# Kernel tuning notes

Measured on AMD Instinct MI355X. Metric: run time of the kernel, lower is better.

The kernel has to match this reference:

```python
import jax, jax.numpy as jnp
import numpy as np

N_NODES = 100000
N_EDGES = 1250000
IN_DIM = 64
HID_DIM = 64
EDGE_DIM = 10
BN_EPS = 1e-5


def setup_inputs() -> dict:
    key = jax.random.key(0)
    ks = jax.random.split(key, 10)
    x = jax.random.normal(ks[0], (N_NODES, IN_DIM), dtype=jnp.float32)
    edge_index = jax.random.randint(ks[1], (2, N_EDGES), 0, N_NODES, dtype=jnp.int64)
    edge_attr = jax.random.normal(ks[2], (N_EDGES, EDGE_DIM), dtype=jnp.float32)
    # GINEConv edge projection Linear(edge_dim=10 -> indim)
    W_edge = jax.random.normal(ks[3], (EDGE_DIM, IN_DIM), dtype=jnp.float32) * (1.0 / np.sqrt(EDGE_DIM))
    b_edge = jnp.zeros((IN_DIM,), dtype=jnp.float32)
    # MLP: Linear(indim, hiddendim) -> ReLU -> Linear(hiddendim, hiddendim)
    W1 = jax.random.normal(ks[4], (IN_DIM, HID_DIM), dtype=jnp.float32) * (1.0 / np.sqrt(IN_DIM))
    b1 = jnp.zeros((HID_DIM,), dtype=jnp.float32)
    W2 = jax.random.normal(ks[5], (HID_DIM, HID_DIM), dtype=jnp.float32) * (1.0 / np.sqrt(HID_DIM))
    b2 = jnp.zeros((HID_DIM,), dtype=jnp.float32)
    # BatchNorm1d affine params
    bn_gamma = jnp.ones((HID_DIM,), dtype=jnp.float32)
    bn_beta = jnp.zeros((HID_DIM,), dtype=jnp.float32)
    return {"x": x, "edge_index": edge_index, "edge_attr": edge_attr,
            "W_edge": W_edge, "b_edge": b_edge, "W1": W1, "b1": b1,
            "W2": W2, "b2": b2, "bn_gamma": bn_gamma, "bn_beta": bn_beta}


def reference(x, edge_index, edge_attr, W_edge, b_edge, W1, b1, W2, b2, bn_gamma, bn_beta):
    src, dst = edge_index[0], edge_index[1]
    # message: ReLU(x_j + lin(edge_attr))  [E, indim]
    msg = jax.nn.relu(x[src] + edge_attr @ W_edge + b_edge)
    # sum-aggregate into destination nodes  [N, indim]
    aggr = jax.ops.segment_sum(msg, dst, num_segments=N_NODES)
    # GIN update: nn((1+eps)*x + aggr), eps=0
    h = x + aggr
    h = jax.nn.relu(h @ W1 + b1) @ W2 + b2
    # outer ReLU then BatchNorm1d (training-mode batch stats)
    h = jax.nn.relu(h)
    mean = jnp.mean(h, axis=0)
    var = jnp.var(h, axis=0)
    out = (h - mean) * jax.lax.rsqrt(var + BN_EPS) * bn_gamma + bn_beta
    return out
```

## Files before the change

kernel.cpp:

```cpp
#include <hip/hip_runtime.h>

#define N_NODES 100000
#define N_EDGES 1250000
#define DIM 64
#define EDGE_DIM 10
#define BN_EPS 1e-5f

#define SCAN_CHUNK 1024
#define NB_SCAN ((N_NODES + SCAN_CHUNK - 1) / SCAN_CHUNK)

#define DEG_OFF    0
#define SUMS_OFF_I (DEG_OFF + N_NODES)
#define OFFS_OFF   (SUMS_OFF_I + 256)
#define CUR_OFF    (OFFS_OFF + N_NODES)
#define BSUM_OFF   (CUR_OFF + N_NODES)
#define WH_OFF     (BSUM_OFF + 128)
#define REC_OFF    (WH_OFF + 4096)

typedef __attribute__((ext_vector_type(8))) short short8v;
typedef __attribute__((ext_vector_type(4))) float f32x4v;

__device__ __forceinline__ unsigned f2bf(float f) {
    unsigned b = __float_as_uint(f);
    return (b + 0x7FFFu + ((b >> 16) & 1u)) >> 16;
}

__device__ __forceinline__ short8v pack8(float4 a, float4 b) {
    short8v r;
    r[0] = (short)f2bf(a.x); r[1] = (short)f2bf(a.y);
    r[2] = (short)f2bf(a.z); r[3] = (short)f2bf(a.w);
    r[4] = (short)f2bf(b.x); r[5] = (short)f2bf(b.y);
    r[6] = (short)f2bf(b.z); r[7] = (short)f2bf(b.w);
    return r;
}

extern "C" __global__ __launch_bounds__(256)
void prep_kernel(const float* __restrict__ x, unsigned short* __restrict__ xh,
                 const int* __restrict__ ei, int* __restrict__ deg)
{
    int t = blockIdx.x * 256 + threadIdx.x;
    int stride = gridDim.x * 256;
    for (int i = t; i < N_NODES * DIM / 4; i += stride) {
        float4 v = ((const float4*)x)[i];
        uint2 p;
        p.x = f2bf(v.x) | (f2bf(v.y) << 16);
        p.y = f2bf(v.z) | (f2bf(v.w) << 16);
        ((uint2*)xh)[i] = p;
    }
    for (int e = t; e < N_EDGES; e += stride) {
        unsigned d = (unsigned)ei[N_EDGES + e];
        d = d < N_NODES ? d : (N_NODES - 1);
        atomicAdd(&deg[d], 1);
    }
}

extern "C" __global__ __launch_bounds__(256)
void scan_bsum_kernel(const int* __restrict__ deg, int* __restrict__ bsum,
                      const float* __restrict__ W1, const float* __restrict__ W2,
                      unsigned* __restrict__ wh)
{
    __shared__ int sw[4];
    int tid = threadIdx.x;
    if (blockIdx.x == 0) {
        for (int g = tid; g < 4096; g += 256) {
            int layer = g >> 11;
            int r  = g & 2047;
            int kb = r >> 10;
            int r2 = r & 1023;
            int cg = r2 >> 8;
            int r3 = r2 & 255;
            int ln = r3 >> 2;
            int ip = r3 & 3;
            int k0 = kb * 32 + (ln >> 4) * 8 + 2 * ip;
            int c  = cg * 16 + (ln & 15);
            const float* W = layer ? W2 : W1;
            unsigned lo = f2bf(W[k0 * DIM + c]);
            unsigned hi = f2bf(W[(k0 + 1) * DIM + c]);
            wh[g] = lo | (hi << 16);
        }
    }
    int base = blockIdx.x * SCAN_CHUNK + tid * 4;
    int s = 0;
    #pragma unroll
    for (int j = 0; j < 4; ++j) {
        int idx = base + j;
        if (idx < N_NODES) s += deg[idx];
    }
    #pragma unroll
    for (int m = 1; m < 64; m <<= 1) s += __shfl_xor(s, m, 64);
    if ((tid & 63) == 0) sw[tid >> 6] = s;
    __syncthreads();
    if (tid == 0) bsum[blockIdx.x] = sw[0] + sw[1] + sw[2] + sw[3];
}

extern "C" __global__ __launch_bounds__(128)
void scan_top_kernel(int* __restrict__ bsum)
{
    __shared__ int s[128];
    int tid = threadIdx.x;
    int v = (tid < NB_SCAN) ? bsum[tid] : 0;
    s[tid] = v;
    __syncthreads();
    #pragma unroll
    for (int off = 1; off < 128; off <<= 1) {
        int t = (tid >= off) ? s[tid - off] : 0;
        __syncthreads();
        s[tid] += t;
        __syncthreads();
    }
    if (tid < NB_SCAN) bsum[tid] = s[tid] - v;
}

extern "C" __global__ __launch_bounds__(256)
void scan_final_kernel(const int* __restrict__ deg, const int* __restrict__ bsum,
                       int* __restrict__ offs, int* __restrict__ cur)
{
    __shared__ int s[256];
    int tid = threadIdx.x;
    int base = blockIdx.x * SCAN_CHUNK + tid * 4;
    int d[4];
    #pragma unroll
    for (int j = 0; j < 4; ++j) {
        int idx = base + j;
        d[j] = (idx < N_NODES) ? deg[idx] : 0;
    }
    int tot = d[0] + d[1] + d[2] + d[3];
    s[tid] = tot;
    __syncthreads();
    #pragma unroll
    for (int off = 1; off < 256; off <<= 1) {
        int t = (tid >= off) ? s[tid - off] : 0;
        __syncthreads();
        s[tid] += t;
        __syncthreads();
    }
    int b = bsum[blockIdx.x] + s[tid] - tot;
    #pragma unroll
    for (int j = 0; j < 4; ++j) {
        int idx = base + j;
        if (idx < N_NODES) { offs[idx] = b; cur[idx] = b; }
        b += d[j];
    }
}

extern "C" __global__ __launch_bounds__(256)
void scatter_kernel(const int* __restrict__ ei, const float* __restrict__ ea,
                    int* __restrict__ cur, int* __restrict__ recs, int fast)
{
    int e = blockIdx.x * 256 + threadIdx.x;
    if (e >= N_EDGES) return;
    unsigned d = (unsigned)ei[N_EDGES + e];
    unsigned s = (unsigned)ei[e];
    d = d < N_NODES ? d : (N_NODES - 1);
    s = s < N_NODES ? s : (N_NODES - 1);
    int pos = atomicAdd(&cur[d], 1);
    if (fast) {
        const float* a = ea + (size_t)e * EDGE_DIM;
        unsigned w[5];
        #pragma unroll
        for (int k = 0; k < 5; ++k) {
            float2 p = *(const float2*)&a[2 * k];
            w[k] = f2bf(p.x) | (f2bf(p.y) << 16);
        }
        int2* r = (int2*)(recs + (size_t)pos * 6);
        r[0] = make_int2((int)s, (int)w[0]);
        r[1] = make_int2((int)w[1], (int)w[2]);
        r[2] = make_int2((int)w[3], (int)w[4]);
    } else {
        ((int2*)recs)[pos] = make_int2((int)s, e);
    }
}

#define SLOT_ACC(W0, Bv, Cv, Xv, MK)                                            \
    {                                                                           \
        float m0 = bias4.x, m1 = bias4.y, m2 = bias4.z, m3 = bias4.w;           \
        unsigned wd_; float a_;                                                 \
        wd_ = (unsigned)(W0);                                                   \
        a_ = __uint_as_float(wd_ << 16);                                        \
        m0 = fmaf(a_, wc[0].x, m0); m1 = fmaf(a_, wc[0].y, m1);                 \
        m2 = fmaf(a_, wc[0].z, m2); m3 = fmaf(a_, wc[0].w, m3);                 \
        a_ = __uint_as_float(wd_ & 0xFFFF0000u);                                \
        m0 = fmaf(a_, wc[1].x, m0); m1 = fmaf(a_, wc[1].y, m1);                 \
        m2 = fmaf(a_, wc[1].z, m2); m3 = fmaf(a_, wc[1].w, m3);                 \
        wd_ = (unsigned)(Bv).x;                                                 \
        a_ = __uint_as_float(wd_ << 16);                                        \
        m0 = fmaf(a_, wc[2].x, m0); m1 = fmaf(a_, wc[2].y, m1);                 \
        m2 = fmaf(a_, wc[2].z, m2); m3 = fmaf(a_, wc[2].w, m3);                 \
        a_ = __uint_as_float(wd_ & 0xFFFF0000u);                                \
        m0 = fmaf(a_, wc[3].x, m0); m1 = fmaf(a_, wc[3].y, m1);                 \
        m2 = fmaf(a_, wc[3].z, m2); m3 = fmaf(a_, wc[3].w, m3);                 \
        wd_ = (unsigned)(Bv).y;                                                 \
        a_ = __uint_as_float(wd_ << 16);                                        \
        m0 = fmaf(a_, wc[4].x, m0); m1 = fmaf(a_, wc[4].y, m1);                 \
        m2 = fmaf(a_, wc[4].z, m2); m3 = fmaf(a_, wc[4].w, m3);                 \
        a_ = __uint_as_float(wd_ & 0xFFFF0000u);                                \
        m0 = fmaf(a_, wc[5].x, m0); m1 = fmaf(a_, wc[5].y, m1);                 \
        m2 = fmaf(a_, wc[5].z, m2); m3 = fmaf(a_, wc[5].w, m3);                 \
        wd_ = (unsigned)(Cv).x;                                                 \
        a_ = __uint_as_float(wd_ << 16);                                        \
        m0 = fmaf(a_, wc[6].x, m0); m1 = fmaf(a_, wc[6].y, m1);                 \
        m2 = fmaf(a_, wc[6].z, m2); m3 = fmaf(a_, wc[6].w, m3);                 \
        a_ = __uint_as_float(wd_ & 0xFFFF0000u);                                \
        m0 = fmaf(a_, wc[7].x, m0); m1 = fmaf(a_, wc[7].y, m1);                 \
        m2 = fmaf(a_, wc[7].z, m2); m3 = fmaf(a_, wc[7].w, m3);                 \
        wd_ = (unsigned)(Cv).y;                                                 \
        a_ = __uint_as_float(wd_ << 16);                                        \
        m0 = fmaf(a_, wc[8].x, m0); m1 = fmaf(a_, wc[8].y, m1);                 \
        m2 = fmaf(a_, wc[8].z, m2); m3 = fmaf(a_, wc[8].w, m3);                 \
        a_ = __uint_as_float(wd_ & 0xFFFF0000u);                                \
        m0 = fmaf(a_, wc[9].x, m0); m1 = fmaf(a_, wc[9].y, m1);                 \
        m2 = fmaf(a_, wc[9].z, m2); m3 = fmaf(a_, wc[9].w, m3);                 \
        float x0_ = __uint_as_float(((unsigned)(Xv).x) << 16);                  \
        float x1_ = __uint_as_float(((unsigned)(Xv).x) & 0xFFFF0000u);          \
        float x2_ = __uint_as_float(((unsigned)(Xv).y) << 16);                  \
        float x3_ = __uint_as_float(((unsigned)(Xv).y) & 0xFFFF0000u);          \
        float c0_ = fmaxf(m0 + x0_, 0.0f);                                      \
        float c1_ = fmaxf(m1 + x1_, 0.0f);                                      \
        float c2_ = fmaxf(m2 + x2_, 0.0f);                                      \
        float c3_ = fmaxf(m3 + x3_, 0.0f);                                      \
        ax += (MK) ? c0_ : 0.0f; ay += (MK) ? c1_ : 0.0f;                       \
        az += (MK) ? c2_ : 0.0f; aw += (MK) ? c3_ : 0.0f;                       \
    }

extern "C" __global__ __launch_bounds__(256)
void aggr_kernel(const unsigned short* __restrict__ xh,
                 const float* __restrict__ ea,
                 const float* __restrict__ We,
                 const float* __restrict__ be,
                 const int* __restrict__ offs,
                 const int* __restrict__ cur,
                 const int* __restrict__ recs,
                 float* __restrict__ aggr,
                 int fast)
{
    int tid  = threadIdx.x;
    int lane = tid & 63;
    int wv   = tid >> 6;
    int fq   = lane & 15;
    int q    = lane >> 4;

    float4 wc[EDGE_DIM];
    #pragma unroll
    for (int k = 0; k < EDGE_DIM; ++k)
        wc[k] = *(const float4*)&We[k * DIM + 4 * fq];
    float4 bias4 = *(const float4*)&be[4 * fq];

    const uint2* xq2 = (const uint2*)xh;
    const int2*  rc2 = (const int2*)recs;

    #pragma unroll 1
    for (int t = 0; t < 2; ++t) {
        int v = blockIdx.x * 8 + wv * 2 + t;
        if (v >= N_NODES) break;
        uint2 sx = xq2[(unsigned)v * 16u + (unsigned)fq];
        int stt = __builtin_amdgcn_readfirstlane(offs[v]);
        int end = __builtin_amdgcn_readfirstlane(cur[v]);
        float ax = 0.f, ay = 0.f, az = 0.f, aw = 0.f;
        int ng = (end - stt + 15) >> 4;
        if (fast) {
            #pragma unroll 1
            for (int g = 0; g < ng; ++g) {
                int i0e = stt + g * 16;
                int e1  = end - 1;
                int s0 = i0e + q, s1 = s0 + 4, s2 = s0 + 8, s3 = s0 + 12;
                int c0 = 3 * min(s0, e1), c1 = 3 * min(s1, e1);
                int c2 = 3 * min(s2, e1), c3 = 3 * min(s3, e1);
                int2 A0 = rc2[c0],     A1 = rc2[c1];
                int2 A2 = rc2[c2],     A3 = rc2[c3];
                int2 B0 = rc2[c0 + 1], C0 = rc2[c0 + 2];
                int2 B1 = rc2[c1 + 1], C1 = rc2[c1 + 2];
                int2 B2 = rc2[c2 + 1], C2 = rc2[c2 + 2];
                int2 B3 = rc2[c3 + 1], C3 = rc2[c3 + 2];
                unsigned u0 = (unsigned)A0.x; u0 = u0 < N_NODES ? u0 : 0u;
                unsigned u1 = (unsigned)A1.x; u1 = u1 < N_NODES ? u1 : 0u;
                unsigned u2 = (unsigned)A2.x; u2 = u2 < N_NODES ? u2 : 0u;
                unsigned u3 = (unsigned)A3.x; u3 = u3 < N_NODES ? u3 : 0u;
                uint2 X0 = xq2[u0 * 16u + (unsigned)fq];
                uint2 X1 = xq2[u1 * 16u + (unsigned)fq];
                uint2 X2 = xq2[u2 * 16u + (unsigned)fq];
                uint2 X3 = xq2[u3 * 16u + (unsigned)fq];
                SLOT_ACC(A0.y, B0, C0, X0, s0 < end);
                SLOT_ACC(A1.y, B1, C1, X1, s1 < end);
                SLOT_ACC(A2.y, B2, C2, X2, s2 < end);
                SLOT_ACC(A3.y, B3, C3, X3, s3 < end);
            }
        } else {
            #pragma unroll 1
            for (int g = 0; g < ng; ++g) {
                int i0e = stt + g * 16;
                int e1  = end - 1;
                int s0 = i0e + q, s1 = s0 + 4, s2 = s0 + 8, s3 = s0 + 12;
                int2 A0 = ((const int2*)recs)[min(s0, e1)];
                int2 A1 = ((const int2*)recs)[min(s1, e1)];
                int2 A2 = ((const int2*)recs)[min(s2, e1)];
                int2 A3 = ((const int2*)recs)[min(s3, e1)];
                unsigned u0 = (unsigned)A0.x; u0 = u0 < N_NODES ? u0 : 0u;
                unsigned u1 = (unsigned)A1.x; u1 = u1 < N_NODES ? u1 : 0u;
                unsigned u2 = (unsigned)A2.x; u2 = u2 < N_NODES ? u2 : 0u;
                unsigned u3 = (unsigned)A3.x; u3 = u3 < N_NODES ? u3 : 0u;
                uint2 X0 = xq2[u0 * 16u + (unsigned)fq];
                uint2 X1 = xq2[u1 * 16u + (unsigned)fq];
                uint2 X2 = xq2[u2 * 16u + (unsigned)fq];
                uint2 X3 = xq2[u3 * 16u + (unsigned)fq];
                #pragma unroll
                for (int p = 0; p < 4; ++p) {
                    int sl = p == 0 ? s0 : p == 1 ? s1 : p == 2 ? s2 : s3;
                    unsigned ue = (unsigned)(p == 0 ? A0.y : p == 1 ? A1.y :
                                             p == 2 ? A2.y : A3.y);
                    ue = ue < N_EDGES ? ue : 0u;
                    uint2 Xv = p == 0 ? X0 : p == 1 ? X1 : p == 2 ? X2 : X3;
                    const float* a = ea + (size_t)ue * EDGE_DIM;
                    float m0 = bias4.x, m1 = bias4.y, m2 = bias4.z, m3 = bias4.w;
                    #pragma unroll
                    for (int k = 0; k < EDGE_DIM; ++k) {
                        float av = a[k];
                        m0 = fmaf(av, wc[k].x, m0);
                        m1 = fmaf(av, wc[k].y, m1);
                        m2 = fmaf(av, wc[k].z, m2);
                        m3 = fmaf(av, wc[k].w, m3);
                    }
                    float x0_ = __uint_as_float(Xv.x << 16);
                    float x1_ = __uint_as_float(Xv.x & 0xFFFF0000u);
                    float x2_ = __uint_as_float(Xv.y << 16);
                    float x3_ = __uint_as_float(Xv.y & 0xFFFF0000u);
                    bool mk = sl < end;
                    ax += mk ? fmaxf(m0 + x0_, 0.f) : 0.f;
                    ay += mk ? fmaxf(m1 + x1_, 0.f) : 0.f;
                    az += mk ? fmaxf(m2 + x2_, 0.f) : 0.f;
                    aw += mk ? fmaxf(m3 + x3_, 0.f) : 0.f;
                }
            }
        }
        ax += __shfl_xor(ax, 16, 64); ax += __shfl_xor(ax, 32, 64);
        ay += __shfl_xor(ay, 16, 64); ay += __shfl_xor(ay, 32, 64);
        az += __shfl_xor(az, 16, 64); az += __shfl_xor(az, 32, 64);
        aw += __shfl_xor(aw, 16, 64); aw += __shfl_xor(aw, 32, 64);
        ax += __uint_as_float(sx.x << 16);
        ay += __uint_as_float(sx.x & 0xFFFF0000u);
        az += __uint_as_float(sx.y << 16);
        aw += __uint_as_float(sx.y & 0xFFFF0000u);
        if (q == 0)
            *(float4*)&aggr[(size_t)v * DIM + 4 * fq] =
                make_float4(ax, ay, az, aw);
    }
}

extern "C" __global__ __launch_bounds__(256)
void mlp_kernel(const unsigned* __restrict__ wh,
                const float* __restrict__ b1,
                const float* __restrict__ b2,
                float* __restrict__ out,
                float* __restrict__ sums)
{
    __shared__ __align__(16) float sY[4][32 * 68];
    __shared__ float sRed[4][2][DIM];

    int tid  = threadIdx.x;
    int lane = tid & 63;
    int wv   = tid >> 6;
    int lr   = lane & 15;
    int kh   = lane >> 4;
    int m0   = blockIdx.x * 128 + wv * 32;

    const int4* whq = (const int4*)wh;

    short8v B1[2][4];
    #pragma unroll
    for (int kb = 0; kb < 2; ++kb)
        #pragma unroll
        for (int cg = 0; cg < 4; ++cg) {
            union { int4 i; short8v s; } u;
            u.i = whq[(kb * 4 + cg) * 64 + lane];
            B1[kb][cg] = u.s;
        }

    short8v A1[2][2];
    #pragma unroll
    for (int rg = 0; rg < 2; ++rg) {
        int row = m0 + rg * 16 + lr;
        row = row < N_NODES ? row : (N_NODES - 1);
        #pragma unroll
        for (int kb = 0; kb < 2; ++kb) {
            const float4* hp =
                (const float4*)&out[(size_t)row * DIM + kb * 32 + kh * 8];
            A1[rg][kb] = pack8(hp[0], hp[1]);
        }
    }

    f32x4v acc1[2][4] = {};
    #pragma unroll
    for (int rg = 0; rg < 2; ++rg)
        #pragma unroll
        for (int cg = 0; cg < 4; ++cg) {
            acc1[rg][cg] = __builtin_amdgcn_mfma_f32_16x16x32_bf16(
                A1[rg][0], B1[0][cg], acc1[rg][cg], 0, 0, 0);
            acc1[rg][cg] = __builtin_amdgcn_mfma_f32_16x16x32_bf16(
                A1[rg][1], B1[1][cg], acc1[rg][cg], 0, 0, 0);
        }

    float* Y = &sY[wv][0];
    #pragma unroll
    for (int cg = 0; cg < 4; ++cg) {
        float bb = b1[cg * 16 + lr];
        #pragma unroll
        for (int rg = 0; rg < 2; ++rg)
            #pragma unroll
            for (int i = 0; i < 4; ++i) {
                float y = fmaxf(acc1[rg][cg][i] + bb, 0.0f);
                Y[(rg * 16 + kh * 4 + i) * 68 + cg * 16 + lr] = y;
            }
    }

    short8v B2[2][4];
    #pragma unroll
    for (int kb = 0; kb < 2; ++kb)
        #pragma unroll
        for (int cg = 0; cg < 4; ++cg) {
            union { int4 i; short8v s; } u;
            u.i = whq[(8 + kb * 4 + cg) * 64 + lane];
            B2[kb][cg] = u.s;
        }

    short8v A2[2][2];
    #pragma unroll
    for (int rg = 0; rg < 2; ++rg)
        #pragma unroll
        for (int kb = 0; kb < 2; ++kb) {
            const float4* yp =
                (const float4*)&Y[(rg * 16 + lr) * 68 + kb * 32 + kh * 8];
            A2[rg][kb] = pack8(yp[0], yp[1]);
        }

    f32x4v acc2[2][4] = {};
    #pragma unroll
    for (int rg = 0; rg < 2; ++rg)
        #pragma unroll
        for (int cg = 0; cg < 4; ++cg) {
            acc2[rg][cg] = __builtin_amdgcn_mfma_f32_16x16x32_bf16(
                A2[rg][0], B2[0][cg], acc2[rg][cg], 0, 0, 0);
            acc2[rg][cg] = __builtin_amdgcn_mfma_f32_16x16x32_bf16(
                A2[rg][1], B2[1][cg], acc2[rg][cg], 0, 0, 0);
        }

    float ps[4] = {0.f, 0.f, 0.f, 0.f};
    float pq[4] = {0.f, 0.f, 0.f, 0.f};
    #pragma unroll
    for (int cg = 0; cg < 4; ++cg) {
        float bb = b2[cg * 16 + lr];
        #pragma unroll
        for (int rg = 0; rg < 2; ++rg)
            #pragma unroll
            for (int i = 0; i < 4; ++i) {
                int node = m0 + rg * 16 + kh * 4 + i;
                float r = fmaxf(acc2[rg][cg][i] + bb, 0.0f);
                if (node < N_NODES) {
                    out[(size_t)node * DIM + cg * 16 + lr] = r;
                    ps[cg] += r;
                    pq[cg] += r * r;
                }
            }
    }
    #pragma unroll
    for (int cg = 0; cg < 4; ++cg) {
        ps[cg] += __shfl_xor(ps[cg], 16, 64);
        ps[cg] += __shfl_xor(ps[cg], 32, 64);
        pq[cg] += __shfl_xor(pq[cg], 16, 64);
        pq[cg] += __shfl_xor(pq[cg], 32, 64);
    }
    if (kh == 0) {
        #pragma unroll
        for (int cg = 0; cg < 4; ++cg) {
            sRed[wv][0][cg * 16 + lr] = ps[cg];
            sRed[wv][1][cg * 16 + lr] = pq[cg];
        }
    }
    __syncthreads();
    if (tid < 128) {
        int f = tid & 63;
        int a = tid >> 6;
        float v = sRed[0][a][f] + sRed[1][a][f] + sRed[2][a][f] + sRed[3][a][f];
        unsafeAtomicAdd(&sums[a * 64 + f], v);
    }
}

extern "C" __global__ __launch_bounds__(256)
void bn_apply_kernel(float* __restrict__ out, const float* __restrict__ sums,
                     const float* __restrict__ gamma, const float* __restrict__ beta)
{
    int j = blockIdx.x * 256 + threadIdx.x;
    int f0 = (j & 15) * 4;
    float4 s1 = *(const float4*)&sums[f0];
    float4 s2 = *(const float4*)&sums[64 + f0];
    float4 gm = *(const float4*)&gamma[f0];
    float4 bt = *(const float4*)&beta[f0];
    const float inv_n = 1.0f / (float)N_NODES;
    float4 sc, sh;
    {
        float m = s1.x * inv_n; float vv = fmaf(-m, m, s2.x * inv_n);
        sc.x = gm.x * rsqrtf(vv + BN_EPS); sh.x = fmaf(-m, sc.x, bt.x);
    }
    {
        float m = s1.y * inv_n; float vv = fmaf(-m, m, s2.y * inv_n);
        sc.y = gm.y * rsqrtf(vv + BN_EPS); sh.y = fmaf(-m, sc.y, bt.y);
    }
    {
        float m = s1.z * inv_n; float vv = fmaf(-m, m, s2.z * inv_n);
        sc.z = gm.z * rsqrtf(vv + BN_EPS); sh.z = fmaf(-m, sc.z, bt.z);
    }
    {
        float m = s1.w * inv_n; float vv = fmaf(-m, m, s2.w * inv_n);
        sc.w = gm.w * rsqrtf(vv + BN_EPS); sh.w = fmaf(-m, sc.w, bt.w);
    }
    float4 v = ((float4*)out)[j];
    v.x = fmaf(v.x, sc.x, sh.x);
    v.y = fmaf(v.y, sc.y, sh.y);
    v.z = fmaf(v.z, sc.z, sh.z);
    v.w = fmaf(v.w, sc.w, sh.w);
    ((float4*)out)[j] = v;
}

extern "C" void kernel_launch(void* const* d_in, const int* in_sizes, int n_in,
                              void* d_out, int out_size, void* d_ws, size_t ws_size,
                              hipStream_t stream)
{
    const float* x     = (const float*)d_in[0];
    const int*   ei    = (const int*)  d_in[1];
    const float* ea    = (const float*)d_in[2];
    const float* We    = (const float*)d_in[3];
    const float* be    = (const float*)d_in[4];
    const float* W1    = (const float*)d_in[5];
    const float* b1    = (const float*)d_in[6];
    const float* W2    = (const float*)d_in[7];
    const float* b2    = (const float*)d_in[8];
    const float* gamma = (const float*)d_in[9];
    const float* beta  = (const float*)d_in[10];

    float* out  = (float*)d_out;
    int*   wsi  = (int*)d_ws;
    int*   deg  = wsi + DEG_OFF;
    float* sums = (float*)(wsi + SUMS_OFF_I);
    int*   offs = wsi + OFFS_OFF;
    int*   cur  = wsi + CUR_OFF;
    int*   bsum = wsi + BSUM_OFF;
    unsigned* wh = (unsigned*)(wsi + WH_OFF);
    int*   recs = wsi + REC_OFF;

    size_t need_fast = ((size_t)REC_OFF + 6u * N_EDGES + (size_t)N_NODES * DIM / 2) * 4u;
    int fast = (ws_size >= need_fast) ? 1 : 0;
    int rec_ints = fast ? 6 * N_EDGES : 2 * N_EDGES;
    unsigned short* xh = (unsigned short*)(wsi + REC_OFF + rec_ints);

    hipMemsetAsync(wsi, 0, (size_t)(N_NODES + 256) * sizeof(int), stream);

    prep_kernel<<<2048, 256, 0, stream>>>(x, xh, ei, deg);
    scan_bsum_kernel<<<NB_SCAN, 256, 0, stream>>>(deg, bsum, W1, W2, wh);
    scan_top_kernel<<<1, 128, 0, stream>>>(bsum);
    scan_final_kernel<<<NB_SCAN, 256, 0, stream>>>(deg, bsum, offs, cur);
    scatter_kernel<<<(N_EDGES + 255) / 256, 256, 0, stream>>>(ei, ea, cur, recs, fast);

    aggr_kernel<<<(N_NODES + 7) / 8, 256, 0, stream>>>(
        xh, ea, We, be, offs, cur, recs, out, fast);

    mlp_kernel<<<(N_NODES + 127) / 128, 256, 0, stream>>>(
        wh, b1, b2, out, sums);

    bn_apply_kernel<<<(N_NODES * DIM / 4) / 256, 256, 0, stream>>>(out, sums, gamma, beta);
}
```

Baseline: 362.9 us.

## Vectorize degree count, fold top scan, nontemporal scatter, coalesce MLP output stores

The degree-count loop now reads destination indices as int4 and issues four atomics per iteration. The separate top-level scan kernel is removed: each scan_final block reduces the preceding block sums itself, which saves one launch at the cost of redundant small reductions. The scatter kernel loads edge attributes before the atomic and writes the records with 64-bit nontemporal stores. The MLP epilogue stages its results in shared memory (Y) and writes them back to out as row-contiguous float4 stores instead of scattered scalar stores.

```diff
diff --git a/kernel.cpp b/kernel.cpp
--- a/kernel.cpp
+++ b/kernel.cpp
@@ -19,6 +19,7 @@
 
 typedef __attribute__((ext_vector_type(8))) short short8v;
 typedef __attribute__((ext_vector_type(4))) float f32x4v;
+typedef unsigned long long ull;
 
 __device__ __forceinline__ unsigned f2bf(float f) {
     unsigned b = __float_as_uint(f);
@@ -47,10 +48,17 @@
         p.y = f2bf(v.z) | (f2bf(v.w) << 16);
         ((uint2*)xh)[i] = p;
     }
-    for (int e = t; e < N_EDGES; e += stride) {
-        unsigned d = (unsigned)ei[N_EDGES + e];
-        d = d < N_NODES ? d : (N_NODES - 1);
-        atomicAdd(&deg[d], 1);
+    const int4* dq = (const int4*)(ei + N_EDGES);
+    for (int i = t; i < N_EDGES / 4; i += stride) {
+        int4 d4 = dq[i];
+        unsigned d0 = (unsigned)d4.x; d0 = d0 < N_NODES ? d0 : (N_NODES - 1);
+        unsigned d1 = (unsigned)d4.y; d1 = d1 < N_NODES ? d1 : (N_NODES - 1);
+        unsigned d2 = (unsigned)d4.z; d2 = d2 < N_NODES ? d2 : (N_NODES - 1);
+        unsigned d3 = (unsigned)d4.w; d3 = d3 < N_NODES ? d3 : (N_NODES - 1);
+        atomicAdd(&deg[d0], 1);
+        atomicAdd(&deg[d1], 1);
+        atomicAdd(&deg[d2], 1);
+        atomicAdd(&deg[d3], 1);
     }
 }
 
@@ -93,30 +101,24 @@
     if (tid == 0) bsum[blockIdx.x] = sw[0] + sw[1] + sw[2] + sw[3];
 }
 
-extern "C" __global__ __launch_bounds__(128)
-void scan_top_kernel(int* __restrict__ bsum)
-{
-    __shared__ int s[128];
-    int tid = threadIdx.x;
-    int v = (tid < NB_SCAN) ? bsum[tid] : 0;
-    s[tid] = v;
-    __syncthreads();
-    #pragma unroll
-    for (int off = 1; off < 128; off <<= 1) {
-        int t = (tid >= off) ? s[tid - off] : 0;
-        __syncthreads();
-        s[tid] += t;
-        __syncthreads();
-    }
-    if (tid < NB_SCAN) bsum[tid] = s[tid] - v;
-}
-
 extern "C" __global__ __launch_bounds__(256)
 void scan_final_kernel(const int* __restrict__ deg, const int* __restrict__ bsum,
                        int* __restrict__ offs, int* __restrict__ cur)
 {
     __shared__ int s[256];
+    __shared__ int sw[4];
+    __shared__ int sbase;
     int tid = threadIdx.x;
+
+    {
+        int v = (tid < blockIdx.x) ? bsum[tid] : 0;
+        #pragma unroll
+        for (int m = 1; m < 64; m <<= 1) v += __shfl_xor(v, m, 64);
+        if ((tid & 63) == 0) sw[tid >> 6] = v;
+        __syncthreads();
+        if (tid == 0) sbase = sw[0] + sw[1] + sw[2] + sw[3];
+    }
+
     int base = blockIdx.x * SCAN_CHUNK + tid * 4;
     int d[4];
     #pragma unroll
@@ -125,6 +127,7 @@
         d[j] = (idx < N_NODES) ? deg[idx] : 0;
     }
     int tot = d[0] + d[1] + d[2] + d[3];
+    __syncthreads();
     s[tid] = tot;
     __syncthreads();
     #pragma unroll
@@ -134,7 +137,7 @@
         s[tid] += t;
         __syncthreads();
     }
-    int b = bsum[blockIdx.x] + s[tid] - tot;
+    int b = sbase + s[tid] - tot;
     #pragma unroll
     for (int j = 0; j < 4; ++j) {
         int idx = base + j;
@@ -153,21 +156,27 @@
     unsigned s = (unsigned)ei[e];
     d = d < N_NODES ? d : (N_NODES - 1);
     s = s < N_NODES ? s : (N_NODES - 1);
-    int pos = atomicAdd(&cur[d], 1);
     if (fast) {
         const float* a = ea + (size_t)e * EDGE_DIM;
-        unsigned w[5];
-        #pragma unroll
-        for (int k = 0; k < 5; ++k) {
-            float2 p = *(const float2*)&a[2 * k];
-            w[k] = f2bf(p.x) | (f2bf(p.y) << 16);
-        }
-        int2* r = (int2*)(recs + (size_t)pos * 6);
-        r[0] = make_int2((int)s, (int)w[0]);
-        r[1] = make_int2((int)w[1], (int)w[2]);
-        r[2] = make_int2((int)w[3], (int)w[4]);
+        float2 p0 = *(const float2*)&a[0];
+        float2 p1 = *(const float2*)&a[2];
+        float2 p2 = *(const float2*)&a[4];
+        float2 p3 = *(const float2*)&a[6];
+        float2 p4 = *(const float2*)&a[8];
+        int pos = atomicAdd(&cur[d], 1);
+        unsigned w0 = f2bf(p0.x) | (f2bf(p0.y) << 16);
+        unsigned w1 = f2bf(p1.x) | (f2bf(p1.y) << 16);
+        unsigned w2 = f2bf(p2.x) | (f2bf(p2.y) << 16);
+        unsigned w3 = f2bf(p3.x) | (f2bf(p3.y) << 16);
+        unsigned w4 = f2bf(p4.x) | (f2bf(p4.y) << 16);
+        ull* r = (ull*)(recs + (size_t)pos * 6);
+        __builtin_nontemporal_store((ull)s  | ((ull)w0 << 32), r);
+        __builtin_nontemporal_store((ull)w1 | ((ull)w2 << 32), r + 1);
+        __builtin_nontemporal_store((ull)w3 | ((ull)w4 << 32), r + 2);
     } else {
-        ((int2*)recs)[pos] = make_int2((int)s, e);
+        int pos = atomicAdd(&cur[d], 1);
+        __builtin_nontemporal_store((ull)s | ((ull)(unsigned)e << 32),
+                                    (ull*)recs + pos);
     }
 }
 
@@ -453,13 +462,27 @@
             for (int i = 0; i < 4; ++i) {
                 int node = m0 + rg * 16 + kh * 4 + i;
                 float r = fmaxf(acc2[rg][cg][i] + bb, 0.0f);
+                Y[(rg * 16 + kh * 4 + i) * 68 + cg * 16 + lr] = r;
                 if (node < N_NODES) {
-                    out[(size_t)node * DIM + cg * 16 + lr] = r;
                     ps[cg] += r;
                     pq[cg] += r * r;
                 }
             }
     }
+
+    {
+        int r0 = lane & 31;
+        int h  = lane >> 5;
+        int node = m0 + r0;
+        if (node < N_NODES) {
+            #pragma unroll
+            for (int j = 0; j < 8; ++j) {
+                float4 vv = *(const float4*)&Y[r0 * 68 + h * 32 + j * 4];
+                *(float4*)&out[(size_t)node * DIM + h * 32 + j * 4] = vv;
+            }
+        }
+    }
+
     #pragma unroll
     for (int cg = 0; cg < 4; ++cg) {
         ps[cg] += __shfl_xor(ps[cg], 16, 64);
@@ -554,7 +577,6 @@
 
     prep_kernel<<<2048, 256, 0, stream>>>(x, xh, ei, deg);
     scan_bsum_kernel<<<NB_SCAN, 256, 0, stream>>>(deg, bsum, W1, W2, wh);
-    scan_top_kernel<<<1, 128, 0, stream>>>(bsum);
     scan_final_kernel<<<NB_SCAN, 256, 0, stream>>>(deg, bsum, offs, cur);
     scatter_kernel<<<(N_EDGES + 255) / 256, 256, 0, stream>>>(ei, ea, cur, recs, fast);
 
```

Measured after the change: 410.9 us. +13.2%, slower.
